# Performance work log

Measured on AMD Instinct MI355X. Metric: run time of the kernel, lower is better.

The kernel has to match this reference:

```python
import jax, jax.numpy as jnp
import numpy as np

EPS = 1e-5  # torch InstanceNorm2d default
C = 512

def setup_inputs() -> dict:
    key = jax.random.key(0)
    ks = jax.random.split(key, 9)
    x = jax.random.normal(ks[0], (4, C, 64, 64), dtype=jnp.float32)
    s = 0.05
    wq = jax.random.normal(ks[1], (C, C), dtype=jnp.float32) * s
    wk = jax.random.normal(ks[2], (C, C), dtype=jnp.float32) * s
    wv = jax.random.normal(ks[3], (C, C), dtype=jnp.float32) * s
    wp = jax.random.normal(ks[4], (C, C), dtype=jnp.float32) * s
    bq = jax.random.normal(ks[5], (C,), dtype=jnp.float32) * s
    bk = jax.random.normal(ks[6], (C,), dtype=jnp.float32) * s
    bv = jax.random.normal(ks[7], (C,), dtype=jnp.float32) * s
    bp = jax.random.normal(ks[8], (C,), dtype=jnp.float32) * s
    return {"x": x, "wq": wq, "bq": bq, "wk": wk, "bk": bk,
            "wv": wv, "bv": bv, "wp": wp, "bp": bp}

def _conv1x1(h, w, b):
    # 1x1 conv == per-pixel channel mixing: (b,c,h,w) x (o,c) -> (b,o,h,w)
    return jnp.einsum('bchw,oc->bohw', h, w) + b[None, :, None, None]

def reference(x, wq, bq, wk, bk, wv, bv, wp, bp):
    b, c, h, w = x.shape
    # InstanceNorm2d (affine=False): normalize each (b,c) plane over spatial dims
    mu = jnp.mean(x, axis=(2, 3), keepdims=True)
    var = jnp.mean(jnp.square(x - mu), axis=(2, 3), keepdims=True)
    hn = (x - mu) * jax.lax.rsqrt(var + EPS)
    q = _conv1x1(hn, wq, bq).reshape(b, c, h * w)
    k = _conv1x1(hn, wk, bk).reshape(b, c, h * w)
    v = _conv1x1(hn, wv, bv).reshape(b, c, h * w)
    # attn[b,i,j] = <q[:, i], k[:, j]> / sqrt(c), softmax over keys j
    attn = jnp.einsum('bci,bcj->bij', q, k) / jnp.sqrt(jnp.asarray(c, x.dtype))
    attn = jax.nn.softmax(attn, axis=2)
    # out[b,c,i] = sum_j v[b,c,j] * attn[b,i,j]
    o = jnp.einsum('bcj,bij->bci', v, attn).reshape(b, c, h, w)
    return x + _conv1x1(o, wp, bp)
```

## Files before the change

### kernel.cpp

```cpp
#include <hip/hip_runtime.h>
#include <hip/hip_bf16.h>

typedef short bf16x8 __attribute__((ext_vector_type(8)));
typedef float f32x4 __attribute__((ext_vector_type(4)));

#define CCH 512
#define NPIX 4096
#define NB 4

__device__ inline unsigned short f2bf(float f) {
  union { __hip_bfloat16 h; unsigned short u; } cv;
  cv.h = __float2bfloat16(f);
  return cv.u;
}

#define GLD16(gp, lp) __builtin_amdgcn_global_load_lds( \
    (const __attribute__((address_space(1))) unsigned int*)(gp), \
    (__attribute__((address_space(3))) unsigned int*)(lp), 16, 0, 0)

__global__ __launch_bounds__(256) void cast_weights_k(
    const float* __restrict__ w0, const float* __restrict__ w1,
    const float* __restrict__ w2, const float* __restrict__ w3,
    unsigned short* __restrict__ out) {
  int z = blockIdx.y;
  const float* src = (z == 0) ? w0 : (z == 1) ? w1 : (z == 2) ? w2 : w3;
  long i = (long)blockIdx.x * 256 + threadIdx.x;
  out[(long)z * CCH * CCH + i] = f2bf(src[i]);
}

__global__ __launch_bounds__(256) void bias_concat_k(
    const float* __restrict__ bq, const float* __restrict__ bk,
    float* __restrict__ bqk) {
  int i = blockIdx.x * 256 + threadIdx.x;
  bqk[i] = (i < CCH) ? bq[i] : bk[i - CCH];
}

__global__ __launch_bounds__(256) void zero_l_k(float* __restrict__ lsum) {
  int i = (blockIdx.x * 256 + threadIdx.x) * 4;
  *(float4*)(lsum + i) = make_float4(0.f, 0.f, 0.f, 0.f);
}

__global__ __launch_bounds__(256) void stats_k(const float* __restrict__ x,
                                               float* __restrict__ stats) {
  long plane = blockIdx.x;
  const float4* p = (const float4*)(x + plane * NPIX);
  int t = threadIdx.x;
  float s = 0.f, q = 0.f;
  for (int c = 0; c < 4; c++) {
    float4 v = p[c * 256 + t];
    s += v.x + v.y + v.z + v.w;
    q += v.x * v.x + v.y * v.y + v.z * v.z + v.w * v.w;
  }
  for (int off = 32; off; off >>= 1) { s += __shfl_xor(s, off); q += __shfl_xor(q, off); }
  __shared__ float rs[4], rq[4];
  int w = t >> 6;
  if ((t & 63) == 0) { rs[w] = s; rq[w] = q; }
  __syncthreads();
  if (t == 0) {
    s = rs[0] + rs[1] + rs[2] + rs[3];
    q = rq[0] + rq[1] + rq[2] + rq[3];
    float mu = s * (1.f / NPIX);
    float var = q * (1.f / NPIX) - mu * mu;
    stats[2 * plane] = mu;
    stats[2 * plane + 1] = rsqrtf(var + 1e-5f);
  }
}

__global__ __launch_bounds__(256) void norm_t_k(const float* __restrict__ x,
                                                const float* __restrict__ stats,
                                                unsigned short* __restrict__ hnT) {
  int b = blockIdx.z;
  int c0 = blockIdx.y * 32, i0 = blockIdx.x * 32;
  __shared__ float tile[32][33];
  int t = threadIdx.x;
  int il = t & 31, cl = t >> 5;
  for (int r = 0; r < 4; r++) {
    int c = c0 + cl + r * 8;
    long pl = (long)b * CCH + c;
    float mu = stats[2 * pl], rsg = stats[2 * pl + 1];
    tile[cl + r * 8][il] = (x[pl * NPIX + i0 + il] - mu) * rsg;
  }
  __syncthreads();
  for (int r = 0; r < 4; r++) {
    int i = i0 + cl + r * 8;
    hnT[((long)b * NPIX + i) * CCH + c0 + il] = f2bf(tile[il][cl + r * 8]);
  }
}

template <int XCDX, int OUTF32, int BIASM, bool RESID, bool SCALE, bool EXPSUM, bool ROWSCALE>
__global__ __launch_bounds__(256) void gemm_bt_k(
    const unsigned short* __restrict__ A, const unsigned short* __restrict__ B,
    void* __restrict__ Cv, const float* __restrict__ bias,
    const float* __restrict__ resid, float* __restrict__ lsum,
    int K, int lda, int ldb, int ldc,
    long sA, long sB, long sC, float scale) {
  int z = blockIdx.z;
  A += z * sA;
  B += z * sB;

  int bx = blockIdx.x, by = blockIdx.y;
  if (XCDX > 0) {
    int s = blockIdx.x + gridDim.x * blockIdx.y;
    int xcd = s & 7, idx = s >> 3;
    int rw = gridDim.x / XCDX;
    int rh = (gridDim.y * XCDX) >> 3;
    int rx0 = (xcd % XCDX) * rw, ry0 = (xcd / XCDX) * rh;
    bx = rx0 + idx % rw;
    by = ry0 + idx / rw;
  }
  const int n0 = bx * 128, m0 = by * 128;

  const int t = threadIdx.x;
  const int lane = t & 63, w = t >> 6;
  const int wr = w >> 1, wc = w & 1;

  __shared__ __align__(16) unsigned short As[128 * 64];
  __shared__ __align__(16) unsigned short Bs[128 * 64];

  f32x4 acc[4][4] = {};

  const int srow = t >> 3;
  const int scol = (((t & 7) ^ (srow & 7)) * 8);
  const unsigned short* ga = A + (long)(m0 + srow) * lda + scol;
  const unsigned short* gb = B + (long)(n0 + srow) * ldb + scol;
  char* lA = (char*)As + t * 16;
  char* lB = (char*)Bs + t * 16;
  const long stpa = (long)32 * lda;
  const long stpb = (long)32 * ldb;

  const int fr = lane & 15, fq = lane >> 4;
  const int chx = fr & 7;
  const unsigned short* rA = As + (wr * 64 + fr) * 64;
  const unsigned short* rB = Bs + (wc * 64 + fr) * 64;

  const int nkt = K >> 6;
  for (int kt = 0; kt < nkt; kt++) {
    const unsigned short* gak = ga + (long)kt * 64;
    const unsigned short* gbk = gb + (long)kt * 64;
    GLD16(gak, lA);
    GLD16(gak + stpa, lA + 4096);
    GLD16(gak + 2 * stpa, lA + 8192);
    GLD16(gak + 3 * stpa, lA + 12288);
    GLD16(gbk, lB);
    GLD16(gbk + stpb, lB + 4096);
    GLD16(gbk + 2 * stpb, lB + 8192);
    GLD16(gbk + 3 * stpb, lB + 12288);
    __syncthreads();
    for (int kk = 0; kk < 2; kk++) {
      const int offA = ((fq + kk * 4) ^ chx) * 8;
      bf16x8 af[4], bfr[4];
      for (int i = 0; i < 4; i++) af[i] = *(const bf16x8*)(rA + i * 1024 + offA);
      for (int i = 0; i < 4; i++) bfr[i] = *(const bf16x8*)(rB + i * 1024 + offA);
      for (int i = 0; i < 4; i++)
        for (int j = 0; j < 4; j++)
          acc[i][j] = __builtin_amdgcn_mfma_f32_16x16x32_bf16(af[i], bfr[j], acc[i][j], 0, 0, 0);
    }
    __syncthreads();
  }

  if (OUTF32) {
    float* Cf = (float*)Cv;
    for (int i = 0; i < 4; i++) {
      int mg = m0 + wr * 64 + i * 16 + fq * 4;
      for (int j = 0; j < 4; j++) {
        int ng = n0 + wc * 64 + j * 16 + fr;
        for (int r = 0; r < 4; r++) {
          float v = acc[i][j][r];
          if (SCALE) v *= scale;
          int m = mg + r;
          if (BIASM == 1) v += bias[m];
          else if (BIASM == 2) v += bias[ng];
          long off = z * sC + (long)m * ldc + ng;
          if (RESID) v += resid[off];
          Cf[off] = v;
        }
      }
    }
  } else {
    float linv[4][4];
    if (ROWSCALE) {
      for (int i = 0; i < 4; i++)
        for (int r = 0; r < 4; r++)
          linv[i][r] = 1.f / lsum[z * NPIX + m0 + wr * 64 + i * 16 + fq * 4 + r];
    }
    float rsum[4][4];
    if (EXPSUM) {
      for (int i = 0; i < 4; i++)
        for (int r = 0; r < 4; r++) rsum[i][r] = 0.f;
    }
    unsigned short* Cb = (unsigned short*)Cv;
    for (int i = 0; i < 4; i++) {
      int mg = m0 + wr * 64 + i * 16 + fq * 4;
      for (int j = 0; j < 4; j++) {
        int ng = n0 + wc * 64 + j * 16 + fr;
        for (int r = 0; r < 4; r++) {
          float v = acc[i][j][r];
          if (SCALE) v *= scale;
          if (BIASM == 1) v += bias[mg + r];
          else if (BIASM == 2) v += bias[ng];
          if (EXPSUM) { v = exp2f(v); rsum[i][r] += v; }
          if (ROWSCALE) v *= linv[i][r];
          Cb[z * sC + (long)(mg + r) * ldc + ng] = f2bf(v);
        }
      }
    }
    if (EXPSUM) {
      for (int i = 0; i < 4; i++)
        for (int r = 0; r < 4; r++) {
          float s = rsum[i][r];
          s += __shfl_xor(s, 1);
          s += __shfl_xor(s, 2);
          s += __shfl_xor(s, 4);
          s += __shfl_xor(s, 8);
          if (fr == 0)
            atomicAdd(&lsum[z * NPIX + m0 + wr * 64 + i * 16 + fq * 4 + r], s);
        }
    }
  }
}

extern "C" void kernel_launch(void* const* d_in, const int* in_sizes, int n_in,
                              void* d_out, int out_size, void* d_ws, size_t ws_size,
                              hipStream_t stream) {
  const float* x  = (const float*)d_in[0];
  const float* wq = (const float*)d_in[1];
  const float* bq = (const float*)d_in[2];
  const float* wk = (const float*)d_in[3];
  const float* bk = (const float*)d_in[4];
  const float* wv = (const float*)d_in[5];
  const float* bv = (const float*)d_in[6];
  const float* wp = (const float*)d_in[7];
  const float* bp = (const float*)d_in[8];

  char* ws = (char*)d_ws;
  const long SLAB = (long)NPIX * CCH;
  const long SLAB2 = (long)NPIX * 1024;
  const long SLABP = (long)NPIX * NPIX;

  float* stats = (float*)ws;
  float* bqk = (float*)(ws + (32l << 10));
  float* lsum = (float*)(ws + (64l << 10));
  unsigned short* wbf = (unsigned short*)(ws + (192l << 10));
  unsigned short* hnT = (unsigned short*)(ws + (192l << 10) + (1l << 21));
  unsigned short* QKt = hnT + 4 * SLAB;
  unsigned short* V   = QKt + 4 * SLAB2;
  unsigned short* Ot  = V + 4 * SLAB;
  unsigned short* S4  = Ot + 4 * SLAB;

  unsigned short* wv_bf = wbf + 2 * 262144;
  unsigned short* wp_bf = wbf + 3 * 262144;

  cast_weights_k<<<dim3(1024, 4, 1), 256, 0, stream>>>(wq, wk, wv, wp, wbf);
  bias_concat_k<<<dim3(4, 1, 1), 256, 0, stream>>>(bq, bk, bqk);
  zero_l_k<<<dim3(16, 1, 1), 256, 0, stream>>>(lsum);
  stats_k<<<dim3(NB * CCH, 1, 1), 256, 0, stream>>>(x, stats);
  norm_t_k<<<dim3(128, 16, 4), 256, 0, stream>>>(x, stats, hnT);

  gemm_bt_k<1, 0, 2, false, false, false, false><<<dim3(8, 32, 4), 256, 0, stream>>>(
      hnT, wbf, QKt, bqk, nullptr, nullptr, 512, 512, 512, 1024, SLAB, 0, SLAB2, 1.f);
  gemm_bt_k<2, 0, 1, false, false, false, false><<<dim3(32, 4, 4), 256, 0, stream>>>(
      wv_bf, hnT, V, bv, nullptr, nullptr, 512, 512, 512, 4096, 0, SLAB, SLAB, 1.f);

  const float isc2 = 0.06375871387551278f;
  gemm_bt_k<2, 0, 0, false, true, true, false><<<dim3(32, 32, 4), 256, 0, stream>>>(
      QKt, QKt + 512, S4, nullptr, nullptr, lsum, 512, 1024, 1024, 4096,
      SLAB2, SLAB2, SLABP, isc2);
  gemm_bt_k<1, 0, 0, false, false, false, true><<<dim3(4, 32, 4), 256, 0, stream>>>(
      S4, V, Ot, nullptr, nullptr, lsum, 4096, 4096, 4096, 512, SLABP, SLAB, SLAB, 1.f);
  gemm_bt_k<2, 1, 1, true, false, false, false><<<dim3(32, 4, 4), 256, 0, stream>>>(
      wp_bf, Ot, d_out, bp, x, nullptr, 512, 512, 512, 4096, 0, SLAB, SLAB, 1.f);
}
```

Before: 307.4 us.

## Add 256x256 tiled 8-wave pipelined GEMM for attention score computation

```diff
diff --git a/kernel.cpp b/kernel.cpp
--- a/kernel.cpp
+++ b/kernel.cpp
@@ -86,6 +86,131 @@
     hnT[((long)b * NPIX + i) * CCH + c0 + il] = f2bf(tile[il][cl + r * 8]);
   }
 }
+
+#define SH(sl, ha, h, kt) do {                                               \
+    const unsigned short* g_ = ((ha) ? gB : gA) + (long)(kt) * 64 +          \
+                               (long)(2 * (h)) * 65536;                      \
+    char* l_ = (char*)LDSu + (sl) * 65536 + (ha) * 32768 + (2 * (h)) * 8192  \
+               + t * 16;                                                     \
+    GLD16(g_, l_);                                                           \
+    GLD16(g_ + 65536, l_ + 8192);                                            \
+  } while (0)
+
+#define PH(sl, qm, qn, WN, SSTMT) do {                                       \
+    if ((WN) == 4) asm volatile("s_waitcnt vmcnt(4)" ::: "memory");          \
+    else if ((WN) == 2) asm volatile("s_waitcnt vmcnt(2)" ::: "memory");     \
+    else if ((WN) == 0) asm volatile("s_waitcnt vmcnt(0)" ::: "memory");     \
+    __builtin_amdgcn_s_barrier();                                            \
+    __builtin_amdgcn_sched_barrier(0);                                       \
+    SSTMT;                                                                   \
+    const unsigned short* sa_ = LDSu + (sl) * 32768;                         \
+    const unsigned short* sb_ = sa_ + 16384;                                 \
+    bf16x8 a_[4][2], b_[2][2];                                               \
+    _Pragma("unroll") for (int mm = 0; mm < 4; mm++) {                       \
+      int row = ((qm) * 4 + mm) * 32 + wr * 16 + fr;                         \
+      a_[mm][0] = *(const bf16x8*)(sa_ + row * 64 + o0_);                    \
+      a_[mm][1] = *(const bf16x8*)(sa_ + row * 64 + o1_);                    \
+    }                                                                        \
+    _Pragma("unroll") for (int nn = 0; nn < 2; nn++) {                       \
+      int row = ((qn) * 2 + nn) * 64 + wc * 16 + fr;                         \
+      b_[nn][0] = *(const bf16x8*)(sb_ + row * 64 + o0_);                    \
+      b_[nn][1] = *(const bf16x8*)(sb_ + row * 64 + o1_);                    \
+    }                                                                        \
+    asm volatile("s_waitcnt lgkmcnt(0)" ::: "memory");                       \
+    __builtin_amdgcn_sched_barrier(0);                                       \
+    __builtin_amdgcn_s_setprio(1);                                           \
+    _Pragma("unroll") for (int mm = 0; mm < 4; mm++)                         \
+      _Pragma("unroll") for (int nn = 0; nn < 2; nn++) {                     \
+        acc[(qm) * 4 + mm][(qn) * 2 + nn] =                                  \
+            __builtin_amdgcn_mfma_f32_16x16x32_bf16(                         \
+                a_[mm][0], b_[nn][0], acc[(qm) * 4 + mm][(qn) * 2 + nn],     \
+                0, 0, 0);                                                    \
+        acc[(qm) * 4 + mm][(qn) * 2 + nn] =                                  \
+            __builtin_amdgcn_mfma_f32_16x16x32_bf16(                         \
+                a_[mm][1], b_[nn][1], acc[(qm) * 4 + mm][(qn) * 2 + nn],     \
+                0, 0, 0);                                                    \
+      }                                                                      \
+    __builtin_amdgcn_s_setprio(0);                                           \
+    __builtin_amdgcn_sched_barrier(0);                                       \
+    __builtin_amdgcn_s_barrier();                                            \
+  } while (0)
+
+__global__ __launch_bounds__(512, 2) void gemm8p_s_k(
+    const unsigned short* __restrict__ A,
+    const unsigned short* __restrict__ B,
+    unsigned short* __restrict__ C,
+    float* __restrict__ lsum, float scale) {
+  const int z = blockIdx.z;
+  const long SLAB2 = (long)NPIX * 1024;
+  const long SLABP = (long)NPIX * NPIX;
+  A += z * SLAB2;
+  B += z * SLAB2;
+  const int m0 = blockIdx.y * 256, n0 = blockIdx.x * 256;
+  const int t = threadIdx.x;
+  const int lane = t & 63, w = t >> 6;
+  const int wr = w >> 2, wc = w & 3;
+  const int fr = lane & 15, fq = lane >> 4;
+  const int chx = fr & 7;
+  const int o0_ = (fq ^ chx) * 8, o1_ = ((fq + 4) ^ chx) * 8;
+
+  __shared__ __align__(16) unsigned short LDSu[2 * 32768];
+
+  f32x4 acc[8][4] = {};
+
+  const int srow = t >> 3;
+  const int scol = ((t & 7) ^ (srow & 7)) * 8;
+  const unsigned short* gA = A + (long)(m0 + srow) * 1024 + scol;
+  const unsigned short* gB = B + (long)(n0 + srow) * 1024 + scol;
+
+  SH(0, 0, 0, 0); SH(0, 1, 0, 0); SH(0, 0, 1, 0); SH(0, 1, 1, 0);
+
+  const int NIT = 4;
+  for (int i = 0; i < NIT - 1; i++) {
+    PH(0, 0, 0, 4, SH(1, 0, 0, 2 * i + 1));
+    PH(0, 0, 1, 2, SH(1, 1, 0, 2 * i + 1));
+    PH(0, 1, 0, -1, SH(1, 0, 1, 2 * i + 1));
+    PH(0, 1, 1, -1, SH(1, 1, 1, 2 * i + 1));
+    PH(1, 0, 0, 4, SH(0, 0, 0, 2 * i + 2));
+    PH(1, 0, 1, 2, SH(0, 1, 0, 2 * i + 2));
+    PH(1, 1, 0, -1, SH(0, 0, 1, 2 * i + 2));
+    PH(1, 1, 1, -1, SH(0, 1, 1, 2 * i + 2));
+  }
+  PH(0, 0, 0, 4, SH(1, 0, 0, 7));
+  PH(0, 0, 1, 2, SH(1, 1, 0, 7));
+  PH(0, 1, 0, -1, SH(1, 0, 1, 7));
+  PH(0, 1, 1, -1, SH(1, 1, 1, 7));
+  PH(1, 0, 0, 4, (void)0);
+  PH(1, 0, 1, 0, (void)0);
+  PH(1, 1, 0, -1, (void)0);
+  PH(1, 1, 1, -1, (void)0);
+
+  float rsum[8][4];
+  for (int i = 0; i < 8; i++)
+    for (int r = 0; r < 4; r++) rsum[i][r] = 0.f;
+  for (int i = 0; i < 8; i++) {
+    int mg = m0 + i * 32 + wr * 16 + fq * 4;
+    for (int j = 0; j < 4; j++) {
+      int ng = n0 + j * 64 + wc * 16 + fr;
+      for (int r = 0; r < 4; r++) {
+        float v = exp2f(acc[i][j][r] * scale);
+        rsum[i][r] += v;
+        C[z * SLABP + (long)(mg + r) * 4096 + ng] = f2bf(v);
+      }
+    }
+  }
+  for (int i = 0; i < 8; i++)
+    for (int r = 0; r < 4; r++) {
+      float s = rsum[i][r];
+      s += __shfl_xor(s, 1);
+      s += __shfl_xor(s, 2);
+      s += __shfl_xor(s, 4);
+      s += __shfl_xor(s, 8);
+      if (fr == 0)
+        atomicAdd(&lsum[z * NPIX + m0 + i * 32 + wr * 16 + fq * 4 + r], s);
+    }
+}
+#undef SH
+#undef PH
 
 template <int XCDX, int OUTF32, int BIASM, bool RESID, bool SCALE, bool EXPSUM, bool ROWSCALE>
 __global__ __launch_bounds__(256) void gemm_bt_k(
@@ -262,9 +387,7 @@
       wv_bf, hnT, V, bv, nullptr, nullptr, 512, 512, 512, 4096, 0, SLAB, SLAB, 1.f);
 
   const float isc2 = 0.06375871387551278f;
-  gemm_bt_k<2, 0, 0, false, true, true, false><<<dim3(32, 32, 4), 256, 0, stream>>>(
-      QKt, QKt + 512, S4, nullptr, nullptr, lsum, 512, 1024, 1024, 4096,
-      SLAB2, SLAB2, SLABP, isc2);
+  gemm8p_s_k<<<dim3(16, 16, 4), 512, 0, stream>>>(QKt, QKt + 512, S4, lsum, isc2);
   gemm_bt_k<1, 0, 0, false, false, false, true><<<dim3(4, 32, 4), 256, 0, stream>>>(
       S4, V, Ot, nullptr, nullptr, lsum, 4096, 4096, 4096, 512, SLABP, SLAB, SLAB, 1.f);
   gemm_bt_k<2, 1, 1, true, false, false, false><<<dim3(32, 4, 4), 256, 0, stream>>>(
```

Result: faster. 301.1 us (-2.1%).
